# Kernel tuning notes

Hardware: AMD Instinct MI355X
Metric: run time of the kernel (lower is better)

The kernel has to match this reference:

```python
import jax, jax.numpy as jnp
import numpy as np

NTYPES = 4
RCUT = 6.0
MIXED_TYPES = False
BOX = 40.0  # Angstrom, sets realistic atomic density


def setup_inputs() -> dict:
    key = jax.random.key(0)
    k1, k2 = jax.random.split(key)
    nframes, nloc = 2, 4096
    coord = jax.random.uniform(k1, (nframes, nloc * 3), dtype=jnp.float32) * BOX
    atype = jax.random.randint(k2, (nframes, nloc), 0, NTYPES, dtype=jnp.int32)
    return {"coord": coord, "atype": atype}


def reference(coord, atype):
    # cell=None branch: extended coords == local coords, nall == nloc
    nframes = coord.shape[0]
    c = coord.reshape(nframes, -1, 3)              # (f, nloc, 3)
    nloc = c.shape[1]
    # diff[f, i, j] = coord[j] - coord[i], shape (f, nloc, nall, 3)
    diff = c[:, None, :, :] - c[:, :, None, :]
    rr2 = jnp.sum(diff * diff, axis=-1)            # (f, nloc, nall)
    # mask self-pairs with inf (torch sets diff rows to inf before squaring)
    eye = jnp.eye(nloc, dtype=bool)
    rr2 = jnp.where(eye[None, :, :], jnp.inf, rr2)
    min_rr2 = jnp.min(rr2, axis=-1)                # (f, nloc)
    mask = rr2 < RCUT ** 2                         # (f, nloc, nall)
    if not MIXED_TYPES:
        # per-type neighbor counts via one-hot contraction (replaces the
        # Python loop over ntypes in the torch code; same math)
        onehot = jax.nn.one_hot(atype, NTYPES, dtype=jnp.int32)  # (f, nall, t)
        nnei = jnp.einsum('fij,fjt->fit', mask.astype(jnp.int32), onehot)
    else:
        valid = (atype >= 0)[:, None, :]
        nnei = jnp.sum(mask & valid, axis=-1).astype(jnp.int32)[..., None]
    max_nnei = jnp.max(nnei, axis=1)               # (f, ntypes) or (f, 1)
    return min_rr2, max_nnei
```

## Files before the change

### kernel.cpp

```cpp
#include <hip/hip_runtime.h>
#include <stdint.h>

#define NFRAMES 2
#define NT 4
#define BLK 256
#define NJ 128
#define IPT 4
#define FBLK 128

template <bool SELFCHK>
__device__ __forceinline__ void do_pair(float cx, float cy, float cz, unsigned sval,
                                        int j, int i,
                                        float xi, float yi, float zi,
                                        float& mm, unsigned& cc) {
#pragma clang fp contract(off)
    float dx = cx - xi;
    float dy = cy - yi;
    float dz = cz - zi;
    float xx = dx * dx;
    float yy = dy * dy;
    float zz = dz * dz;
    float r2 = (xx + yy) + zz;
    bool self = SELFCHK && (j == i);
    mm = fminf(mm, self ? __builtin_inff() : r2);
    bool near = (r2 < 36.0f) && !self;
    cc += near ? sval : 0u;
}

template <bool SELFCHK>
__device__ __forceinline__ void pair_body(const float* __restrict__ cf,
                                          const int* __restrict__ tf,
                                          int jbase, int jslice,
                                          const int (&ii)[IPT],
                                          const float (&xi)[IPT],
                                          const float (&yi)[IPT],
                                          const float (&zi)[IPT],
                                          float (&ma)[IPT], float (&mb)[IPT],
                                          unsigned (&ca)[IPT], unsigned (&cb)[IPT]) {
#pragma unroll 4
    for (int j = jbase; j < jbase + jslice; j += 2) {
        float cx0 = cf[3 * j], cy0 = cf[3 * j + 1], cz0 = cf[3 * j + 2];
        unsigned s0 = 1u << (tf[j] * 8);
#pragma unroll
        for (int k = 0; k < IPT; ++k)
            do_pair<SELFCHK>(cx0, cy0, cz0, s0, j, ii[k], xi[k], yi[k], zi[k], ma[k], ca[k]);
        float cx1 = cf[3 * j + 3], cy1 = cf[3 * j + 4], cz1 = cf[3 * j + 5];
        unsigned s1 = 1u << (tf[j + 1] * 8);
#pragma unroll
        for (int k = 0; k < IPT; ++k)
            do_pair<SELFCHK>(cx1, cy1, cz1, s1, j + 1, ii[k], xi[k], yi[k], zi[k], mb[k], cb[k]);
    }
}

__global__ __launch_bounds__(BLK) void ns_pair_kernel(const float* __restrict__ coord,
                                                      const int* __restrict__ atype,
                                                      uint2* __restrict__ part,
                                                      float* __restrict__ out,
                                                      int nloc) {
    const int f = blockIdx.z;
    const int q = nloc >> 2;
    const int ib = blockIdx.y * BLK;
    const int jslice = nloc / NJ;
    const int jb = blockIdx.x;
    const int jbase = jb * jslice;

    if (blockIdx.x == 0 && blockIdx.y == 0 && blockIdx.z == 0 &&
        threadIdx.x < NFRAMES * NT)
        ((unsigned*)out)[(size_t)NFRAMES * nloc + threadIdx.x] = 0u;

    const float* cf = coord + (size_t)f * nloc * 3;
    const int*   tf = atype + (size_t)f * nloc;

    int ii[IPT];
    float xi[IPT], yi[IPT], zi[IPT];
    float ma[IPT], mb[IPT];
    unsigned ca[IPT], cb[IPT];
    bool ov = false;
#pragma unroll
    for (int k = 0; k < IPT; ++k) {
        const int base = ib + k * q;
        ii[k] = base + threadIdx.x;
        xi[k] = cf[3 * ii[k]];
        yi[k] = cf[3 * ii[k] + 1];
        zi[k] = cf[3 * ii[k] + 2];
        ma[k] = mb[k] = __builtin_inff();
        ca[k] = cb[k] = 0u;
        ov |= (jbase >= base) && (jbase < base + BLK);
    }

    if (ov)
        pair_body<true >(cf, tf, jbase, jslice, ii, xi, yi, zi, ma, mb, ca, cb);
    else
        pair_body<false>(cf, tf, jbase, jslice, ii, xi, yi, zi, ma, mb, ca, cb);

    const size_t pb = ((size_t)jb * NFRAMES + f) * nloc;
#pragma unroll
    for (int k = 0; k < IPT; ++k)
        part[pb + ii[k]] = make_uint2(__float_as_uint(fminf(ma[k], mb[k])), ca[k] + cb[k]);
}

__global__ __launch_bounds__(FBLK) void ns_finalize_kernel(const uint2* __restrict__ part,
                                                           float* __restrict__ out,
                                                           int nloc) {
    const int nbpf = nloc / FBLK;
    const int f = blockIdx.x / nbpf;
    const int i = (blockIdx.x % nbpf) * FBLK + threadIdx.x;

    float ma = __builtin_inff(), mb = __builtin_inff();
    unsigned cacc = 0u, cbacc = 0u;
#pragma unroll 8
    for (int jb = 0; jb < NJ; jb += 2) {
        uint2 va = part[((size_t)jb * NFRAMES + f) * nloc + i];
        uint2 vb = part[((size_t)(jb + 1) * NFRAMES + f) * nloc + i];
        ma = fminf(ma, __uint_as_float(va.x));
        mb = fminf(mb, __uint_as_float(vb.x));
        cacc += va.y;
        cbacc += vb.y;
    }
    out[(size_t)f * nloc + i] = fminf(ma, mb);
    const unsigned c = cacc + cbacc;

    int m0 = (int)(c & 255u);
    int m1 = (int)((c >> 8) & 255u);
    int m2 = (int)((c >> 16) & 255u);
    int m3 = (int)(c >> 24);
    for (int off = 32; off > 0; off >>= 1) {
        m0 = max(m0, __shfl_xor(m0, off, 64));
        m1 = max(m1, __shfl_xor(m1, off, 64));
        m2 = max(m2, __shfl_xor(m2, off, 64));
        m3 = max(m3, __shfl_xor(m3, off, 64));
    }
    __shared__ int red[FBLK / 64][NT];
    const int wid = threadIdx.x >> 6;
    if ((threadIdx.x & 63) == 0) {
        red[wid][0] = m0; red[wid][1] = m1; red[wid][2] = m2; red[wid][3] = m3;
    }
    __syncthreads();
    if (threadIdx.x < NT) {
        const int t = threadIdx.x;
        const int m = max(red[0][t], red[1][t]);
        atomicMax((unsigned*)out + (size_t)NFRAMES * nloc + f * NT + t,
                  __float_as_uint((float)m));
    }
}

extern "C" void kernel_launch(void* const* d_in, const int* in_sizes, int n_in,
                              void* d_out, int out_size, void* d_ws, size_t ws_size,
                              hipStream_t stream) {
    const float* coord = (const float*)d_in[0];
    const int*   atype = (const int*)d_in[1];
    const int nloc = in_sizes[1] / NFRAMES;

    float* out  = (float*)d_out;
    uint2* part = (uint2*)d_ws;

    dim3 grid(NJ, nloc / (BLK * IPT), NFRAMES);
    ns_pair_kernel<<<grid, dim3(BLK), 0, stream>>>(coord, atype, part, out, nloc);

    const int nbpf = nloc / FBLK;
    ns_finalize_kernel<<<NFRAMES * nbpf, FBLK, 0, stream>>>(part, out, nloc);
}
```

Baseline: 26.52 us.

## Broadcast j-slice coordinates via readlane and halve j-split count

Each lane now loads one j atom's coordinates and type, and the wave broadcasts them with readlane instead of every thread issuing scalar/global loads per j. The j-split count drops from 128 to 64, so each block handles 64 j atoms, which matches one wave, and fewer partial results are written and reduced. The aim is to cut redundant j-coordinate loads and finalize traffic. The cost is fewer blocks for parallelism and readlane instructions inside the inner loop. The code hardcodes a slice of 64 j atoms, so it is only correct while nloc/NJ equals 64.

Measured after the change: 24.21 us. 1.1x faster.

```diff
diff --git a/kernel.cpp b/kernel.cpp
--- a/kernel.cpp
+++ b/kernel.cpp
@@ -4,9 +4,13 @@
 #define NFRAMES 2
 #define NT 4
 #define BLK 256
-#define NJ 128
+#define NJ 64
 #define IPT 4
 #define FBLK 128
+
+__device__ __forceinline__ float bcast_f(float v, int l) {
+    return __uint_as_float(__builtin_amdgcn_readlane(__float_as_uint(v), l));
+}
 
 template <bool SELFCHK>
 __device__ __forceinline__ void do_pair(float cx, float cy, float cz, unsigned sval,
@@ -28,27 +32,27 @@
 }
 
 template <bool SELFCHK>
-__device__ __forceinline__ void pair_body(const float* __restrict__ cf,
-                                          const int* __restrict__ tf,
-                                          int jbase, int jslice,
-                                          const int (&ii)[IPT],
-                                          const float (&xi)[IPT],
-                                          const float (&yi)[IPT],
-                                          const float (&zi)[IPT],
-                                          float (&ma)[IPT], float (&mb)[IPT],
-                                          unsigned (&ca)[IPT], unsigned (&cb)[IPT]) {
-#pragma unroll 4
-    for (int j = jbase; j < jbase + jslice; j += 2) {
-        float cx0 = cf[3 * j], cy0 = cf[3 * j + 1], cz0 = cf[3 * j + 2];
-        unsigned s0 = 1u << (tf[j] * 8);
+__device__ __forceinline__ void chunk_loop(float bx, float by, float bz, unsigned bs,
+                                           int jbase,
+                                           const int (&ii)[IPT],
+                                           const float (&xi)[IPT],
+                                           const float (&yi)[IPT],
+                                           const float (&zi)[IPT],
+                                           float (&mA)[IPT], float (&mB)[IPT],
+                                           unsigned (&cA)[IPT], unsigned (&cB)[IPT]) {
+#pragma unroll 8
+    for (int l = 0; l < 64; l += 2) {
+        float cx0 = bcast_f(bx, l), cy0 = bcast_f(by, l), cz0 = bcast_f(bz, l);
+        unsigned s0 = __builtin_amdgcn_readlane(bs, l);
+        const int j0 = jbase + l;
 #pragma unroll
         for (int k = 0; k < IPT; ++k)
-            do_pair<SELFCHK>(cx0, cy0, cz0, s0, j, ii[k], xi[k], yi[k], zi[k], ma[k], ca[k]);
-        float cx1 = cf[3 * j + 3], cy1 = cf[3 * j + 4], cz1 = cf[3 * j + 5];
-        unsigned s1 = 1u << (tf[j + 1] * 8);
+            do_pair<SELFCHK>(cx0, cy0, cz0, s0, j0, ii[k], xi[k], yi[k], zi[k], mA[k], cA[k]);
+        float cx1 = bcast_f(bx, l + 1), cy1 = bcast_f(by, l + 1), cz1 = bcast_f(bz, l + 1);
+        unsigned s1 = __builtin_amdgcn_readlane(bs, l + 1);
 #pragma unroll
         for (int k = 0; k < IPT; ++k)
-            do_pair<SELFCHK>(cx1, cy1, cz1, s1, j + 1, ii[k], xi[k], yi[k], zi[k], mb[k], cb[k]);
+            do_pair<SELFCHK>(cx1, cy1, cz1, s1, j0 + 1, ii[k], xi[k], yi[k], zi[k], mB[k], cB[k]);
     }
 }
 
@@ -58,23 +62,25 @@
                                                       float* __restrict__ out,
                                                       int nloc) {
     const int f = blockIdx.z;
-    const int q = nloc >> 2;
+    const int q = nloc / IPT;
     const int ib = blockIdx.y * BLK;
-    const int jslice = nloc / NJ;
-    const int jb = blockIdx.x;
-    const int jbase = jb * jslice;
+    const int jbase = blockIdx.x * (nloc / NJ);
 
-    if (blockIdx.x == 0 && blockIdx.y == 0 && blockIdx.z == 0 &&
-        threadIdx.x < NFRAMES * NT)
+    if (blockIdx.x == 0 && blockIdx.y == 0 && f == 0 && threadIdx.x < NFRAMES * NT)
         ((unsigned*)out)[(size_t)NFRAMES * nloc + threadIdx.x] = 0u;
 
     const float* cf = coord + (size_t)f * nloc * 3;
     const int*   tf = atype + (size_t)f * nloc;
 
+    const int lane = threadIdx.x & 63;
+    const int jl = jbase + lane;
+    const float bx = cf[3 * jl], by = cf[3 * jl + 1], bz = cf[3 * jl + 2];
+    const unsigned bs = 1u << (tf[jl] * 8);
+
     int ii[IPT];
     float xi[IPT], yi[IPT], zi[IPT];
-    float ma[IPT], mb[IPT];
-    unsigned ca[IPT], cb[IPT];
+    float mA[IPT], mB[IPT];
+    unsigned cA[IPT], cB[IPT];
     bool ov = false;
 #pragma unroll
     for (int k = 0; k < IPT; ++k) {
@@ -83,20 +89,20 @@
         xi[k] = cf[3 * ii[k]];
         yi[k] = cf[3 * ii[k] + 1];
         zi[k] = cf[3 * ii[k] + 2];
-        ma[k] = mb[k] = __builtin_inff();
-        ca[k] = cb[k] = 0u;
+        mA[k] = mB[k] = __builtin_inff();
+        cA[k] = cB[k] = 0u;
         ov |= (jbase >= base) && (jbase < base + BLK);
     }
 
     if (ov)
-        pair_body<true >(cf, tf, jbase, jslice, ii, xi, yi, zi, ma, mb, ca, cb);
+        chunk_loop<true >(bx, by, bz, bs, jbase, ii, xi, yi, zi, mA, mB, cA, cB);
     else
-        pair_body<false>(cf, tf, jbase, jslice, ii, xi, yi, zi, ma, mb, ca, cb);
+        chunk_loop<false>(bx, by, bz, bs, jbase, ii, xi, yi, zi, mA, mB, cA, cB);
 
-    const size_t pb = ((size_t)jb * NFRAMES + f) * nloc;
+    const size_t pb = ((size_t)blockIdx.x * NFRAMES + f) * nloc;
 #pragma unroll
     for (int k = 0; k < IPT; ++k)
-        part[pb + ii[k]] = make_uint2(__float_as_uint(fminf(ma[k], mb[k])), ca[k] + cb[k]);
+        part[pb + ii[k]] = make_uint2(__float_as_uint(fminf(mA[k], mB[k])), cA[k] + cB[k]);
 }
 
 __global__ __launch_bounds__(FBLK) void ns_finalize_kernel(const uint2* __restrict__ part,
```
